# Optimization experiments

Measured on AMD Instinct MI355X. Metric: run time of the kernel, lower is better.

Reference implementation:

```python
import jax, jax.numpy as jnp
import numpy as np
from jax import lax

LRELU_SLOPE = 0.2
GAIN = 2.0 ** 0.5
EPS = 1e-8


def setup_inputs() -> dict:
    key = jax.random.key(0)
    ks = jax.random.split(key, 8)
    B, NDW, CIN, COUT, H, W = 4, 512, 16, 16, 1024, 1024
    return {
        "w": jax.random.normal(ks[0], (B, NDW), jnp.float32),
        "x": jax.random.normal(ks[1], (B, CIN, H, W), jnp.float32),
        "noise": jax.random.normal(ks[2], (B, 1, H, W), jnp.float32),
        "fc_weight": jax.random.normal(ks[3], (CIN, NDW), jnp.float32),
        "fc_bias": jnp.ones((CIN,), jnp.float32),
        "conv_weight": jax.random.normal(ks[4], (COUT, CIN, 3, 3), jnp.float32),
        "conv_bias": jax.random.normal(ks[5], (COUT,), jnp.float32),
        "scale_noise": jnp.float32(0.1),
    }


def reference(w, x, noise, fc_weight, fc_bias, conv_weight, conv_bias, scale_noise):
    NDW = fc_weight.shape[1]
    COUT, CIN, KH, KW = conv_weight.shape
    # equal_lr scaling (FC): weight * n_dim_in**-0.5
    s = w @ (fc_weight.T * (NDW ** -0.5)) + fc_bias  # [B, CIN] style per input channel
    # equal_lr scaling (Conv): weight * (in_channels * k^2)**-0.5
    wc = conv_weight * ((CIN * KH * KW) ** -0.5)  # [COUT, CIN, 3, 3]
    # demodulation coefficient: d[b,o] = 1/sqrt(sum_{i,kh,kw} (s[b,i]*wc[o,i,kh,kw])^2 + eps)
    w2 = (wc ** 2).sum(axis=(2, 3))  # [COUT, CIN]
    d = lax.rsqrt((s ** 2) @ w2.T + EPS)  # [B, COUT]
    # modulate input instead of materializing per-sample weights (mathematically identical)
    xm = x * s[:, :, None, None]
    y = lax.conv_general_dilated(
        xm, wc, window_strides=(1, 1), padding=((1, 1), (1, 1)),
        dimension_numbers=("NCHW", "OIHW", "NCHW"))
    y = y * d[:, :, None, None] + conv_bias[None, :, None, None]
    y = y + scale_noise * noise  # broadcast noise over channels
    y = GAIN * jnp.where(y >= 0, y, LRELU_SLOPE * y)
    return (w, y)
```

## Files before the change

kernel.cpp:

```cpp
#include <hip/hip_runtime.h>

#define H_ 1024
#define W_ 1024
#define B_ 4
#define CIN 16
#define COUT 16
#define TH 8
#define TW 64
#define LDS_COLS 66
#define LDS_ROWS 10
#define PIX_STRIDE 24

#define LRELU 0.2f
#define GAIN_ 1.4142135623730951f
#define EPS_ 1e-8f

typedef __attribute__((ext_vector_type(8))) short bf16x8;
typedef __attribute__((ext_vector_type(4))) float f32x4;

static __device__ __forceinline__ unsigned short f32_to_bf16(float f) {
    unsigned int u = __float_as_uint(f);
    unsigned int r = u + 0x7FFF + ((u >> 16) & 1);
    return (unsigned short)(r >> 16);
}

__global__ __launch_bounds__(256) void k_setup1(
    const float* __restrict__ w, const float* __restrict__ fcw,
    const float* __restrict__ fcb, float* __restrict__ s_out,
    float* __restrict__ w_copy_out)
{
    __shared__ float part[256];
    const int tid = threadIdx.x;
    const int bi = tid >> 2;
    const int q  = tid & 3;
    const int b = bi >> 4, i = bi & 15;
    const float* wr = w + b * 512 + q * 128;
    const float* fr = fcw + i * 512 + q * 128;
    float acc = 0.f;
    #pragma unroll 8
    for (int k = 0; k < 128; ++k) acc += wr[k] * fr[k];
    part[tid] = acc;
    __syncthreads();
    if (tid < 64) {
        float v = part[tid*4] + part[tid*4+1] + part[tid*4+2] + part[tid*4+3];
        s_out[tid] = v * 0.04419417382415922f  + fcb[tid & 15];
    }
    for (int e = tid; e < B_ * 512; e += 256) w_copy_out[e] = w[e];
}

__global__ __launch_bounds__(256) void k_setup2(
    const float* __restrict__ s_in, const float* __restrict__ convw,
    unsigned short* __restrict__ afrag)
{
    const int b = blockIdx.x;
    const int tid = threadIdx.x;
    __shared__ float s_sh[16];
    __shared__ float d_sh[16];
    __shared__ float wc_sh[COUT * CIN * 9];
    __shared__ float part[256];

    if (tid < 16) s_sh[tid] = s_in[b * 16 + tid];
    for (int e = tid; e < COUT * CIN * 9; e += 256)
        wc_sh[e] = convw[e] * (1.0f / 12.0f);
    __syncthreads();

    const int o = tid >> 4, i = tid & 15;
    const float si = s_sh[i];
    float acc = 0.f;
    #pragma unroll
    for (int tap = 0; tap < 9; ++tap) {
        float v = wc_sh[(o * 16 + i) * 9 + tap] * si;
        acc += v * v;
    }
    part[tid] = acc;
    __syncthreads();
    if (tid < 16) {
        float sum = EPS_;
        #pragma unroll
        for (int j = 0; j < 16; ++j) sum += part[tid * 16 + j];
        d_sh[tid] = rsqrtf(sum);
    }
    __syncthreads();

    for (int e = tid; e < 5 * 64 * 8; e += 256) {
        int t = e >> 9;
        int lane = (e >> 3) & 63;
        int j = e & 7;
        int oo = lane & 15, g = lane >> 4;
        int ii = (g & 1) * 8 + j;
        int tap = 2 * t + (g >> 1);
        float v = 0.f;
        if (tap < 9) v = wc_sh[(oo * 16 + ii) * 9 + tap] * s_sh[ii] * d_sh[oo];
        afrag[(size_t)b * (5 * 64 * 8) + e] = f32_to_bf16(v);
    }
}

__global__ __launch_bounds__(256) void k_conv(
    const float* __restrict__ x, const float* __restrict__ noise,
    const float* __restrict__ conv_bias, const float* __restrict__ sn_ptr,
    const unsigned short* __restrict__ afrag, float* __restrict__ y)
{
    __shared__ unsigned short tile[LDS_ROWS * LDS_COLS * PIX_STRIDE];

    const int tid = threadIdx.x;
    const int bt = blockIdx.z;
    const int h0 = blockIdx.y * TH;
    const int w0 = blockIdx.x * TW;
    const float sn = sn_ptr[0];

    {
        const float* xb = x + (size_t)bt * CIN * H_ * W_;
        for (int ve = tid; ve < CIN * LDS_ROWS * 16; ve += 256) {
            int ch  = ve / (LDS_ROWS * 16);
            int rem = ve % (LDS_ROWS * 16);
            int row = rem >> 4;
            int col = 1 + ((rem & 15) << 2);
            int gh = h0 - 1 + row;
            float4 v = make_float4(0.f, 0.f, 0.f, 0.f);
            if (gh >= 0 && gh < H_)
                v = *reinterpret_cast<const float4*>(
                        xb + ((size_t)ch * H_ + gh) * W_ + (w0 - 1 + col));
            unsigned short* dst = &tile[(row * LDS_COLS + col) * PIX_STRIDE + ch];
            dst[0]              = f32_to_bf16(v.x);
            dst[PIX_STRIDE]     = f32_to_bf16(v.y);
            dst[2 * PIX_STRIDE] = f32_to_bf16(v.z);
            dst[3 * PIX_STRIDE] = f32_to_bf16(v.w);
        }
        for (int e = tid; e < CIN * LDS_ROWS * 2; e += 256) {
            int ch  = e / (LDS_ROWS * 2);
            int rem = e % (LDS_ROWS * 2);
            int row = rem >> 1;
            int col = (rem & 1) * (LDS_COLS - 1);
            int gh = h0 - 1 + row;
            int gw = w0 - 1 + col;
            float v = 0.f;
            if (gh >= 0 && gh < H_ && gw >= 0 && gw < W_)
                v = xb[((size_t)ch * H_ + gh) * W_ + gw];
            tile[(row * LDS_COLS + col) * PIX_STRIDE + ch] = f32_to_bf16(v);
        }
    }

    const int lane  = tid & 63;
    const int wid   = tid >> 6;
    const int p     = lane & 15;
    const int g     = lane >> 4;
    const int ghalf = g >> 1;
    const int chalf = g & 1;

    bf16x8 a[5];
    {
        const bf16x8* ap =
            reinterpret_cast<const bf16x8*>(afrag + (size_t)bt * 5 * 64 * 8);
        #pragma unroll
        for (int t = 0; t < 5; ++t) a[t] = ap[t * 64 + lane];
    }
    float bias_j[4];
    #pragma unroll
    for (int j = 0; j < 4; ++j) bias_j[j] = conv_bias[g * 4 + j];

    int lroff[5], lcoff[5];
    #pragma unroll
    for (int t = 0; t < 5; ++t) {
        int tap = 2 * t + ghalf;
        if (tap > 8) tap = 8;
        lroff[t] = tap / 3;
        lcoff[t] = tap % 3;
    }

    __syncthreads();

    float* yb = y + (size_t)bt * COUT * H_ * W_;
    const float* nb = noise + (size_t)bt * H_ * W_;

    #pragma unroll
    for (int rr = 0; rr < 2; ++rr) {
        const int oh = wid * 2 + rr;
        #pragma unroll
        for (int gc = 0; gc < 4; ++gc) {
            const int ow = gc * 16;
            f32x4 acc = {0.f, 0.f, 0.f, 0.f};
            #pragma unroll
            for (int t = 0; t < 5; ++t) {
                const unsigned short* src =
                    &tile[((oh + lroff[t]) * LDS_COLS + (ow + p + lcoff[t])) * PIX_STRIDE
                          + chalf * 8];
                bf16x8 bv = *reinterpret_cast<const bf16x8*>(src);
                acc = __builtin_amdgcn_mfma_f32_16x16x32_bf16(a[t], bv, acc, 0, 0, 0);
            }
            const int gh = h0 + oh;
            const int gw = w0 + ow + p;
            const float noi = nb[(size_t)gh * W_ + gw] * sn;
            #pragma unroll
            for (int j = 0; j < 4; ++j) {
                float v = acc[j] + bias_j[j] + noi;
                v = (v >= 0.f) ? v : (LRELU * v);
                yb[((size_t)(g * 4 + j) * H_ + gh) * W_ + gw] = v * GAIN_;
            }
        }
    }
}

extern "C" void kernel_launch(void* const* d_in, const int* in_sizes, int n_in,
                              void* d_out, int out_size, void* d_ws, size_t ws_size,
                              hipStream_t stream)
{
    const float* w     = (const float*)d_in[0];
    const float* x     = (const float*)d_in[1];
    const float* noise = (const float*)d_in[2];
    const float* fcw   = (const float*)d_in[3];
    const float* fcb   = (const float*)d_in[4];
    const float* convw = (const float*)d_in[5];
    const float* convb = (const float*)d_in[6];
    const float* sn    = (const float*)d_in[7];

    float* out = (float*)d_out;
    float* ws_s = (float*)d_ws;
    unsigned short* ws_afrag = (unsigned short*)((char*)d_ws + 256);

    k_setup1<<<1, 256, 0, stream>>>(w, fcw, fcb, ws_s, out);
    k_setup2<<<B_, 256, 0, stream>>>(ws_s, convw, ws_afrag);
    dim3 grid(W_ / TW, H_ / TH, B_);
    k_conv<<<grid, 256, 0, stream>>>(x, noise, convb, sn, ws_afrag, out + 2048);
}
```

Measured before the change: 204.9 us.

## Split LDS tile into channel-half planes and pack bf16x8 stores per pixel

Changes the shared-memory tile from a padded per-pixel stride of 24 channels to two planes of 8 channels each, so every pixel holds a contiguous 16-byte bf16x8. The fill loop is reorganized so 160 threads each load eight channel rows as float4, transpose them in registers and write packed 16-byte LDS stores, with 20 threads handling the halo columns. This replaces many scalar 2-byte LDS writes and shrinks the LDS footprint. The cost is that only 180 of 256 threads do loading, plus higher register pressure from holding eight float4s, and the new 16-byte stride may bring different bank-conflict behavior on the MFMA operand reads.

Result: faster. 181.3 us (-11.5%).

```diff
diff --git a/kernel.cpp b/kernel.cpp
--- a/kernel.cpp
+++ b/kernel.cpp
@@ -9,7 +9,6 @@
 #define TW 64
 #define LDS_COLS 66
 #define LDS_ROWS 10
-#define PIX_STRIDE 24
 
 #define LRELU 0.2f
 #define GAIN_ 1.4142135623730951f
@@ -100,43 +99,61 @@
     const float* __restrict__ conv_bias, const float* __restrict__ sn_ptr,
     const unsigned short* __restrict__ afrag, float* __restrict__ y)
 {
-    __shared__ unsigned short tile[LDS_ROWS * LDS_COLS * PIX_STRIDE];
+    __shared__ unsigned short tile[2][LDS_ROWS][LDS_COLS][8];
 
     const int tid = threadIdx.x;
     const int bt = blockIdx.z;
     const int h0 = blockIdx.y * TH;
     const int w0 = blockIdx.x * TW;
     const float sn = sn_ptr[0];
-
-    {
-        const float* xb = x + (size_t)bt * CIN * H_ * W_;
-        for (int ve = tid; ve < CIN * LDS_ROWS * 16; ve += 256) {
-            int ch  = ve / (LDS_ROWS * 16);
-            int rem = ve % (LDS_ROWS * 16);
-            int row = rem >> 4;
-            int col = 1 + ((rem & 15) << 2);
-            int gh = h0 - 1 + row;
-            float4 v = make_float4(0.f, 0.f, 0.f, 0.f);
-            if (gh >= 0 && gh < H_)
-                v = *reinterpret_cast<const float4*>(
-                        xb + ((size_t)ch * H_ + gh) * W_ + (w0 - 1 + col));
-            unsigned short* dst = &tile[(row * LDS_COLS + col) * PIX_STRIDE + ch];
-            dst[0]              = f32_to_bf16(v.x);
-            dst[PIX_STRIDE]     = f32_to_bf16(v.y);
-            dst[2 * PIX_STRIDE] = f32_to_bf16(v.z);
-            dst[3 * PIX_STRIDE] = f32_to_bf16(v.w);
+    const float* xb = x + (size_t)bt * CIN * H_ * W_;
+
+    if (tid < 160) {
+        const int row = tid >> 4;
+        const int cg  = tid & 15;
+        const int gh  = h0 - 1 + row;
+        const bool okr = (gh >= 0) && (gh < H_);
+        #pragma unroll
+        for (int h = 0; h < 2; ++h) {
+            float4 v[8];
+            #pragma unroll
+            for (int c = 0; c < 8; ++c) {
+                v[c] = make_float4(0.f, 0.f, 0.f, 0.f);
+                if (okr)
+                    v[c] = *reinterpret_cast<const float4*>(
+                        xb + ((size_t)(8 * h + c) * H_ + gh) * W_ + (w0 + 4 * cg));
+            }
+            #pragma unroll
+            for (int px = 0; px < 4; ++px) {
+                bf16x8 pk;
+                pk[0] = (short)f32_to_bf16(px == 0 ? v[0].x : px == 1 ? v[0].y : px == 2 ? v[0].z : v[0].w);
+                pk[1] = (short)f32_to_bf16(px == 0 ? v[1].x : px == 1 ? v[1].y : px == 2 ? v[1].z : v[1].w);
+                pk[2] = (short)f32_to_bf16(px == 0 ? v[2].x : px == 1 ? v[2].y : px == 2 ? v[2].z : v[2].w);
+                pk[3] = (short)f32_to_bf16(px == 0 ? v[3].x : px == 1 ? v[3].y : px == 2 ? v[3].z : v[3].w);
+                pk[4] = (short)f32_to_bf16(px == 0 ? v[4].x : px == 1 ? v[4].y : px == 2 ? v[4].z : v[4].w);
+                pk[5] = (short)f32_to_bf16(px == 0 ? v[5].x : px == 1 ? v[5].y : px == 2 ? v[5].z : v[5].w);
+                pk[6] = (short)f32_to_bf16(px == 0 ? v[6].x : px == 1 ? v[6].y : px == 2 ? v[6].z : v[6].w);
+                pk[7] = (short)f32_to_bf16(px == 0 ? v[7].x : px == 1 ? v[7].y : px == 2 ? v[7].z : v[7].w);
+                *reinterpret_cast<bf16x8*>(&tile[h][row][1 + 4 * cg + px][0]) = pk;
+            }
         }
-        for (int e = tid; e < CIN * LDS_ROWS * 2; e += 256) {
-            int ch  = e / (LDS_ROWS * 2);
-            int rem = e % (LDS_ROWS * 2);
-            int row = rem >> 1;
-            int col = (rem & 1) * (LDS_COLS - 1);
-            int gh = h0 - 1 + row;
-            int gw = w0 - 1 + col;
-            float v = 0.f;
-            if (gh >= 0 && gh < H_ && gw >= 0 && gw < W_)
-                v = xb[((size_t)ch * H_ + gh) * W_ + gw];
-            tile[(row * LDS_COLS + col) * PIX_STRIDE + ch] = f32_to_bf16(v);
+    } else if (tid < 180) {
+        const int u    = tid - 160;
+        const int row  = u >> 1;
+        const int side = u & 1;
+        const int col  = side * (LDS_COLS - 1);
+        const int gh   = h0 - 1 + row;
+        const int gw   = w0 - 1 + col;
+        const bool ok  = (gh >= 0) && (gh < H_) && (gw >= 0) && (gw < W_);
+        #pragma unroll
+        for (int h = 0; h < 2; ++h) {
+            bf16x8 pk;
+            #pragma unroll
+            for (int c = 0; c < 8; ++c) {
+                float v = ok ? xb[((size_t)(8 * h + c) * H_ + gh) * W_ + gw] : 0.f;
+                pk[c] = (short)f32_to_bf16(v);
+            }
+            *reinterpret_cast<bf16x8*>(&tile[h][row][col][0]) = pk;
         }
     }
 
@@ -181,10 +198,8 @@
             f32x4 acc = {0.f, 0.f, 0.f, 0.f};
             #pragma unroll
             for (int t = 0; t < 5; ++t) {
-                const unsigned short* src =
-                    &tile[((oh + lroff[t]) * LDS_COLS + (ow + p + lcoff[t])) * PIX_STRIDE
-                          + chalf * 8];
-                bf16x8 bv = *reinterpret_cast<const bf16x8*>(src);
+                const bf16x8 bv = *reinterpret_cast<const bf16x8*>(
+                    &tile[chalf][oh + lroff[t]][ow + p + lcoff[t]][0]);
                 acc = __builtin_amdgcn_mfma_f32_16x16x32_bf16(a[t], bv, acc, 0, 0, 0);
             }
             const int gh = h0 + oh;
```

## Drop LDS staging in conv kernel and gather MFMA operands directly from global

Applied to the files above, without the earlier changes.

Removes the shared-memory tile and its barrier from the convolution kernel. Each wave now handles one output row and builds its bf16 B-fragments with scalar global loads per tap and channel, relying on the L1/L2 caches for the halo reuse. This removes the LDS transpose/convert stage and the synchronisation cost, but adds many uncoalesced, redundant global loads (about 9x reuse now served by cache) and halves the rows per block.

Measured after the change: 375.4 us. 83.2% more time.

```diff
diff --git a/kernel.cpp b/kernel.cpp
--- a/kernel.cpp
+++ b/kernel.cpp
@@ -2,14 +2,11 @@
 
 #define H_ 1024
 #define W_ 1024
+#define HW_ (H_ * W_)
 #define B_ 4
 #define CIN 16
 #define COUT 16
-#define TH 8
 #define TW 64
-#define LDS_COLS 66
-#define LDS_ROWS 10
-#define PIX_STRIDE 24
 
 #define LRELU 0.2f
 #define GAIN_ 1.4142135623730951f
@@ -100,57 +97,26 @@
     const float* __restrict__ conv_bias, const float* __restrict__ sn_ptr,
     const unsigned short* __restrict__ afrag, float* __restrict__ y)
 {
-    __shared__ unsigned short tile[LDS_ROWS * LDS_COLS * PIX_STRIDE];
-
-    const int tid = threadIdx.x;
-    const int bt = blockIdx.z;
-    const int h0 = blockIdx.y * TH;
-    const int w0 = blockIdx.x * TW;
-    const float sn = sn_ptr[0];
-
-    {
-        const float* xb = x + (size_t)bt * CIN * H_ * W_;
-        for (int ve = tid; ve < CIN * LDS_ROWS * 16; ve += 256) {
-            int ch  = ve / (LDS_ROWS * 16);
-            int rem = ve % (LDS_ROWS * 16);
-            int row = rem >> 4;
-            int col = 1 + ((rem & 15) << 2);
-            int gh = h0 - 1 + row;
-            float4 v = make_float4(0.f, 0.f, 0.f, 0.f);
-            if (gh >= 0 && gh < H_)
-                v = *reinterpret_cast<const float4*>(
-                        xb + ((size_t)ch * H_ + gh) * W_ + (w0 - 1 + col));
-            unsigned short* dst = &tile[(row * LDS_COLS + col) * PIX_STRIDE + ch];
-            dst[0]              = f32_to_bf16(v.x);
-            dst[PIX_STRIDE]     = f32_to_bf16(v.y);
-            dst[2 * PIX_STRIDE] = f32_to_bf16(v.z);
-            dst[3 * PIX_STRIDE] = f32_to_bf16(v.w);
-        }
-        for (int e = tid; e < CIN * LDS_ROWS * 2; e += 256) {
-            int ch  = e / (LDS_ROWS * 2);
-            int rem = e % (LDS_ROWS * 2);
-            int row = rem >> 1;
-            int col = (rem & 1) * (LDS_COLS - 1);
-            int gh = h0 - 1 + row;
-            int gw = w0 - 1 + col;
-            float v = 0.f;
-            if (gh >= 0 && gh < H_ && gw >= 0 && gw < W_)
-                v = xb[((size_t)ch * H_ + gh) * W_ + gw];
-            tile[(row * LDS_COLS + col) * PIX_STRIDE + ch] = f32_to_bf16(v);
-        }
-    }
-
-    const int lane  = tid & 63;
-    const int wid   = tid >> 6;
+    const int tid  = threadIdx.x;
+    const int bt   = blockIdx.z;
+    const int wid  = tid >> 6;
+    const int lane = tid & 63;
+    const int gh   = blockIdx.y * 4 + wid;
+    const int w0   = blockIdx.x * TW;
     const int p     = lane & 15;
     const int g     = lane >> 4;
     const int ghalf = g >> 1;
     const int chalf = g & 1;
+    const float sn = sn_ptr[0];
+
+    const float* xb = x + (size_t)bt * CIN * HW_;
+    const float* xh = xb + (size_t)(chalf * 8) * HW_;
+    float* yb = y + (size_t)bt * COUT * HW_;
+    const float* nb = noise + (size_t)bt * HW_;
 
     bf16x8 a[5];
     {
-        const bf16x8* ap =
-            reinterpret_cast<const bf16x8*>(afrag + (size_t)bt * 5 * 64 * 8);
+        const bf16x8* ap = reinterpret_cast<const bf16x8*>(afrag + (size_t)bt * 5 * 64 * 8);
         #pragma unroll
         for (int t = 0; t < 5; ++t) a[t] = ap[t * 64 + lane];
     }
@@ -167,35 +133,39 @@
         lcoff[t] = tap % 3;
     }
 
-    __syncthreads();
-
-    float* yb = y + (size_t)bt * COUT * H_ * W_;
-    const float* nb = noise + (size_t)bt * H_ * W_;
+    float nv[4];
+    #pragma unroll
+    for (int gc = 0; gc < 4; ++gc)
+        nv[gc] = nb[(size_t)gh * W_ + w0 + gc * 16 + p];
 
     #pragma unroll
-    for (int rr = 0; rr < 2; ++rr) {
-        const int oh = wid * 2 + rr;
+    for (int gc = 0; gc < 4; ++gc) {
+        const int ow = gc * 16;
+        f32x4 acc = {0.f, 0.f, 0.f, 0.f};
         #pragma unroll
-        for (int gc = 0; gc < 4; ++gc) {
-            const int ow = gc * 16;
-            f32x4 acc = {0.f, 0.f, 0.f, 0.f};
+        for (int tt = 0; tt < 5; ++tt) {
+            const int ghx = gh + lroff[tt] - 1;
+            const int gwx = w0 + ow + p + lcoff[tt] - 1;
+            const bool ok = ((unsigned)ghx < (unsigned)H_) && ((unsigned)gwx < (unsigned)W_);
+            const int ghc = ok ? ghx : gh;
+            const int gwc = ok ? gwx : (w0 + ow + p);
+            const float* src = xh + (size_t)ghc * W_ + gwc;
+            bf16x8 bv;
             #pragma unroll
-            for (int t = 0; t < 5; ++t) {
-                const unsigned short* src =
-                    &tile[((oh + lroff[t]) * LDS_COLS + (ow + p + lcoff[t])) * PIX_STRIDE
-                          + chalf * 8];
-                bf16x8 bv = *reinterpret_cast<const bf16x8*>(src);
-                acc = __builtin_amdgcn_mfma_f32_16x16x32_bf16(a[t], bv, acc, 0, 0, 0);
+            for (int j = 0; j < 8; ++j) {
+                float v = src[(size_t)j * HW_];
+                v = ok ? v : 0.f;
+                bv[j] = (short)f32_to_bf16(v);
             }
-            const int gh = h0 + oh;
-            const int gw = w0 + ow + p;
-            const float noi = nb[(size_t)gh * W_ + gw] * sn;
-            #pragma unroll
-            for (int j = 0; j < 4; ++j) {
-                float v = acc[j] + bias_j[j] + noi;
-                v = (v >= 0.f) ? v : (LRELU * v);
-                yb[((size_t)(g * 4 + j) * H_ + gh) * W_ + gw] = v * GAIN_;
-            }
+            acc = __builtin_amdgcn_mfma_f32_16x16x32_bf16(a[tt], bv, acc, 0, 0, 0);
+        }
+        const int gw = w0 + ow + p;
+        const float noi = nv[gc] * sn;
+        #pragma unroll
+        for (int j = 0; j < 4; ++j) {
+            float vv = acc[j] + bias_j[j] + noi;
+            vv = (vv >= 0.f) ? vv : (LRELU * vv);
+            yb[((size_t)(g * 4 + j) * H_ + gh) * W_ + gw] = vv * GAIN_;
         }
     }
 }
@@ -219,6 +189,6 @@
 
     k_setup1<<<1, 256, 0, stream>>>(w, fcw, fcb, ws_s, out);
     k_setup2<<<B_, 256, 0, stream>>>(ws_s, convw, ws_afrag);
-    dim3 grid(W_ / TW, H_ / TH, B_);
+    dim3 grid(W_ / TW, H_ / 4, B_);
     k_conv<<<grid, 256, 0, stream>>>(x, noise, convb, sn, ws_afrag, out + 2048);
 }
```
